# Kernel optimization log

Measured on AMD Instinct MI355X. Metric: run time of the kernel, lower is better.

Reference implementation:

```python
import jax, jax.numpy as jnp
import numpy as np

H = 12   # num_attention_heads
T = 8    # sample_num (frames)
D = 768  # hidden_size


def ln(x, g, b, eps=1e-12):
    m = x.mean(-1, keepdims=True)
    v = x.var(-1, keepdims=True)
    return (x - m) / jnp.sqrt(v + eps) * g + b


def attn(q, k, v):
    # q: [..., Q, Dh], k/v: [..., K, Dh]
    d = q.shape[-1]
    s = jnp.einsum('...qd,...kd->...qk', q, k) / jnp.sqrt(jnp.asarray(d, q.dtype))
    a = jax.nn.softmax(s, axis=-1)
    return jnp.einsum('...qk,...kd->...qd', a, v)


def mha_divided(x, Wq, bq, Wk, bk, Wv, bv, Wo, bo, mode):
    B, S, Dm = x.shape
    Dh = Dm // H
    P = (S - 1) // T

    def proj(W, b):
        return (x @ W + b).reshape(B, S, H, Dh).transpose(0, 2, 1, 3)  # [B,H,S,Dh]

    q, k, v = proj(Wq, bq), proj(Wk, bk), proj(Wv, bv)

    # cls token attends over the full sequence
    cls_ctx = attn(q[:, :, 0:1], k, v)                       # [B,H,1,Dh]
    cls_out = cls_ctx.transpose(0, 2, 1, 3).reshape(B, 1, Dm) @ Wo + bo

    qp = q[:, :, 1:].reshape(B, H, T, P, Dh)
    kp = k[:, :, 1:].reshape(B, H, T, P, Dh)
    vp = v[:, :, 1:].reshape(B, H, T, P, Dh)
    kc, vc = k[:, :, 0], v[:, :, 0]                          # [B,H,Dh]

    if mode == 'time':
        # each patch attends over [cls] + same patch across T frames
        qt = qp.transpose(0, 1, 3, 2, 4)                     # [B,H,P,T,Dh]
        kt = jnp.concatenate([jnp.broadcast_to(kc[:, :, None, None], (B, H, P, 1, Dh)),
                              kp.transpose(0, 1, 3, 2, 4)], axis=3)  # [B,H,P,T+1,Dh]
        vt = jnp.concatenate([jnp.broadcast_to(vc[:, :, None, None], (B, H, P, 1, Dh)),
                              vp.transpose(0, 1, 3, 2, 4)], axis=3)
        ctx = attn(qt, kt, vt)                               # [B,H,P,T,Dh]
        out = ctx.transpose(0, 3, 2, 1, 4).reshape(B, T * P, Dm)  # [B,T,P,H,Dh]
    else:  # 'space': each frame attends over [cls] + P patches in that frame
        kt = jnp.concatenate([jnp.broadcast_to(kc[:, :, None, None], (B, H, T, 1, Dh)), kp], axis=3)
        vt = jnp.concatenate([jnp.broadcast_to(vc[:, :, None, None], (B, H, T, 1, Dh)), vp], axis=3)
        ctx = attn(qp, kt, vt)                               # [B,H,T,P,Dh]
        out = ctx.transpose(0, 2, 3, 1, 4).reshape(B, T * P, Dm)
    out = out @ Wo + bo
    return jnp.concatenate([cls_out, out], axis=1)


def _forward(hidden_states,
             t_Wq, t_bq, t_Wk, t_bk, t_Wv, t_bv, t_Wo, t_bo,
             s_Wq, s_bq, s_Wk, s_bk, s_Wv, s_bv, s_Wo, s_bo,
             W1, b1, W2, b2,
             ln1_g, ln1_b, ln2_g, ln2_b, ln3_g, ln3_b):
    x = hidden_states
    # divided time attention
    x = x + mha_divided(ln(x, ln1_g, ln1_b), t_Wq, t_bq, t_Wk, t_bk, t_Wv, t_bv, t_Wo, t_bo, 'time')
    # divided space attention
    x = x + mha_divided(ln(x, ln2_g, ln2_b), s_Wq, s_bq, s_Wk, s_bk, s_Wv, s_bv, s_Wo, s_bo, 'space')
    # feed-forward with exact (erf) GELU
    h = ln(x, ln3_g, ln3_b)
    x = x + jax.nn.gelu(h @ W1 + b1, approximate=False) @ W2 + b2
    return x


def setup_inputs() -> dict:
    key = jax.random.key(0)
    ks = jax.random.split(key, 16)

    def w(k, shape, s=0.02):
        return jax.random.normal(k, shape, jnp.float32) * s

    B, S = 8, 1 + T * 196
    inp = {"hidden_states": jax.random.normal(ks[0], (B, S, D), jnp.float32)}
    names = ["t_Wq", "t_Wk", "t_Wv", "t_Wo", "s_Wq", "s_Wk", "s_Wv", "s_Wo"]
    for i, n in enumerate(names):
        inp[n] = w(ks[1 + i], (D, D))
        inp[n.replace("W", "b")] = jnp.zeros((D,), jnp.float32)
    inp["W1"] = w(ks[9], (D, 4 * D)); inp["b1"] = jnp.zeros((4 * D,), jnp.float32)
    inp["W2"] = w(ks[10], (4 * D, D)); inp["b2"] = jnp.zeros((D,), jnp.float32)
    for i in (1, 2, 3):
        inp[f"ln{i}_g"] = jnp.ones((D,), jnp.float32)
        inp[f"ln{i}_b"] = jnp.zeros((D,), jnp.float32)
    return inp


def reference(hidden_states,
              t_Wq, t_bq, t_Wk, t_bk, t_Wv, t_bv, t_Wo, t_bo,
              s_Wq, s_bq, s_Wk, s_bk, s_Wv, s_bv, s_Wo, s_bo,
              W1, b1, W2, b2,
              ln1_g, ln1_b, ln2_g, ln2_b, ln3_g, ln3_b):
    return _forward(hidden_states,
                    t_Wq, t_bq, t_Wk, t_bk, t_Wv, t_bv, t_Wo, t_bo,
                    s_Wq, s_bq, s_Wk, s_bk, s_Wv, s_bv, s_Wo, s_bo,
                    W1, b1, W2, b2,
                    ln1_g, ln1_b, ln2_g, ln2_b, ln3_g, ln3_b)
```

## Files before the change

### kernel.cpp

```cpp
#include <hip/hip_runtime.h>

#define BQ   8
#define SQ   1569
#define BS   12552
#define DM   768
#define NH   12
#define DH   64
#define TT   8
#define PP   196
#define D4   3072
#define QKVN 2304
#define CCH  24
#define CKEY 66
#define MB_PAD 104

typedef _Float16 f16;
typedef _Float16 f16x8 __attribute__((ext_vector_type(8)));
typedef float    f32x4 __attribute__((ext_vector_type(4)));
typedef unsigned long long u64;

#define AS1 __attribute__((address_space(1)))
#define AS3 __attribute__((address_space(3)))

#define Y_OFF    0ULL
#define QKV_OFF  19279872ULL
#define CTX_OFF  77119488ULL
#define H_OFF    19279872ULL
#define W_OFF    96399360ULL

__global__ __launch_bounds__(256) void ln_kernel(const float* __restrict__ x,
                                                 const float* __restrict__ g,
                                                 const float* __restrict__ bta,
                                                 f16* __restrict__ y) {
    int row = blockIdx.x * 4 + (threadIdx.x >> 6);
    int lane = threadIdx.x & 63;
    if (row >= BS) return;
    const float* xr = x + (u64)row * DM;
    float v[12];
    float s = 0.f, s2 = 0.f;
#pragma unroll
    for (int i = 0; i < 12; i++) { v[i] = xr[lane + i * 64]; s += v[i]; s2 += v[i] * v[i]; }
#pragma unroll
    for (int m = 1; m < 64; m <<= 1) { s += __shfl_xor(s, m, 64); s2 += __shfl_xor(s2, m, 64); }
    float mean = s * (1.f / 768.f);
    float var  = s2 * (1.f / 768.f) - mean * mean;
    float rstd = rsqrtf(var + 1e-12f);
    f16* yr = y + (u64)row * DM;
#pragma unroll
    for (int i = 0; i < 12; i++) {
        int c = lane + i * 64;
        yr[c] = (f16)((v[i] - mean) * rstd * g[c] + bta[c]);
    }
}

__global__ __launch_bounds__(256) void transpose_kernel(const float* __restrict__ src,
                                                        f16* __restrict__ dst,
                                                        int R, int C) {
    __shared__ float tile[32][33];
    int bx = blockIdx.x * 32;
    int by = blockIdx.y * 32;
    int tx = threadIdx.x & 31, ty = threadIdx.x >> 5;
#pragma unroll
    for (int i = 0; i < 4; i++) {
        int r = by + ty + i * 8, c = bx + tx;
        if (r < R && c < C) tile[ty + i * 8][tx] = src[(u64)r * C + c];
    }
    __syncthreads();
#pragma unroll
    for (int i = 0; i < 4; i++) {
        int c = bx + ty + i * 8, r = by + tx;
        if (c < C && r < R) dst[(u64)c * R + r] = (f16)tile[tx][ty + i * 8];
    }
}

__global__ __launch_bounds__(256) void bias3_kernel(const float* __restrict__ a,
                                                    const float* __restrict__ b,
                                                    const float* __restrict__ c,
                                                    float* __restrict__ dst) {
    int i = blockIdx.x * 256 + threadIdx.x;
    if (i < 768) { dst[i] = a[i]; dst[i + 768] = b[i]; dst[i + 1536] = c[i]; }
}

template <int NOUT, bool GELU, bool RESID, bool OUTF16>
__global__ __launch_bounds__(256, 5) void gemm_kernel(const f16* __restrict__ A,
                                                      const f16* __restrict__ Bt,
                                                      const float* __restrict__ bias,
                                                      const float* __restrict__ resid,
                                                      float* __restrict__ Cf,
                                                      f16* __restrict__ Ch,
                                                      int K) {
    __shared__ __align__(16) f16 As[2][128 * 32];
    __shared__ __align__(16) f16 Bs[2][128 * 32];
    int id = blockIdx.x;
    int mb = id % MB_PAD, nb = id / MB_PAD;
    if (mb >= 99) return;
    int tid  = threadIdx.x;
    int lane = tid & 63, wave = tid >> 6;
    int wm = wave >> 1, wn = wave & 1;
    int m0 = mb * 128, n0 = nb * 128;
    int l15 = lane & 15, quad = lane >> 4;

    int r0   = wave * 16 + (lane >> 2);
    int coff = (lane & 3) * 8;
    const f16* ag0 = A + (u64)(m0 + r0) * K + coff;
    const f16* ag1 = A + (u64)(m0 + r0 + 64) * K + coff;
    bool av0 = (m0 + r0) < BS, av1 = (m0 + r0 + 64) < BS;
    const f16* bg0 = Bt + (u64)(n0 + r0) * K + coff;
    const f16* bg1 = Bt + (u64)(n0 + r0 + 64) * K + coff;
    int lofs = wave * 1024;

    f32x4 acc[4][4];
#pragma unroll
    for (int i = 0; i < 4; i++)
#pragma unroll
        for (int j = 0; j < 4; j++)
#pragma unroll
            for (int r = 0; r < 4; r++) acc[i][j][r] = 0.f;

    if (av0) __builtin_amdgcn_global_load_lds((const AS1 void*)ag0, (AS3 void*)((AS3 char*)&As[0][0] + lofs), 16, 0, 0);
    if (av1) __builtin_amdgcn_global_load_lds((const AS1 void*)ag1, (AS3 void*)((AS3 char*)&As[0][0] + lofs + 4096), 16, 0, 0);
    __builtin_amdgcn_global_load_lds((const AS1 void*)bg0, (AS3 void*)((AS3 char*)&Bs[0][0] + lofs), 16, 0, 0);
    __builtin_amdgcn_global_load_lds((const AS1 void*)bg1, (AS3 void*)((AS3 char*)&Bs[0][0] + lofs + 4096), 16, 0, 0);
    ag0 += 32; ag1 += 32; bg0 += 32; bg1 += 32;

    int nit = K >> 5;
    for (int it = 0; it < nit; it++) {
        __syncthreads();
        int buf = it & 1;
        if (it + 1 < nit) {
            int nb2 = buf ^ 1;
            if (av0) __builtin_amdgcn_global_load_lds((const AS1 void*)ag0, (AS3 void*)((AS3 char*)&As[nb2][0] + lofs), 16, 0, 0);
            if (av1) __builtin_amdgcn_global_load_lds((const AS1 void*)ag1, (AS3 void*)((AS3 char*)&As[nb2][0] + lofs + 4096), 16, 0, 0);
            __builtin_amdgcn_global_load_lds((const AS1 void*)bg0, (AS3 void*)((AS3 char*)&Bs[nb2][0] + lofs), 16, 0, 0);
            __builtin_amdgcn_global_load_lds((const AS1 void*)bg1, (AS3 void*)((AS3 char*)&Bs[nb2][0] + lofs + 4096), 16, 0, 0);
            ag0 += 32; ag1 += 32; bg0 += 32; bg1 += 32;
        }
        f16x8 af[4], bf[4];
#pragma unroll
        for (int i = 0; i < 4; i++)
            af[i] = *(const f16x8*)(&As[buf][(wm * 64 + i * 16 + l15) * 32 + quad * 8]);
#pragma unroll
        for (int j = 0; j < 4; j++)
            bf[j] = *(const f16x8*)(&Bs[buf][(wn * 64 + j * 16 + l15) * 32 + quad * 8]);
#pragma unroll
        for (int i = 0; i < 4; i++)
#pragma unroll
            for (int j = 0; j < 4; j++)
                acc[i][j] = __builtin_amdgcn_mfma_f32_16x16x32_f16(af[i], bf[j], acc[i][j], 0, 0, 0);
    }

#pragma unroll
    for (int i = 0; i < 4; i++) {
#pragma unroll
        for (int j = 0; j < 4; j++) {
            int col = n0 + wn * 64 + j * 16 + l15;
            float bv = bias[col];
#pragma unroll
            for (int r = 0; r < 4; r++) {
                int row = m0 + wm * 64 + i * 16 + quad * 4 + r;
                if (row < BS) {
                    float v = acc[i][j][r] + bv;
                    if (GELU) {
                        float u = 0.7978845608028654f * (v + 0.044715f * v * v * v);
                        float e = __builtin_exp2f(-2.885390081777927f * u);
                        v = v / (1.f + e);
                    }
                    if (RESID) v += resid[(u64)row * NOUT + col];
                    if (OUTF16) Ch[(u64)row * NOUT + col] = (f16)v;
                    else        Cf[(u64)row * NOUT + col] = v;
                }
            }
        }
    }
}

__global__ __launch_bounds__(256) void time_attn_kernel(const f16* __restrict__ qkv,
                                                        f16* __restrict__ ctx) {
    int w = blockIdx.x * 4 + (threadIdx.x >> 6);
    int lane = threadIdx.x & 63;
    int b = w / (NH * PP);
    int rem = w % (NH * PP);
    int h = rem / PP, p = rem % PP;
    u64 bb = (u64)b * SQ;
    int hoff = h * 64 + lane;

    float qv[TT], kv[9], vv[9];
#pragma unroll
    for (int t = 0; t < TT; t++) qv[t] = (float)qkv[(bb + 1 + t * PP + p) * QKVN + hoff];
    kv[0] = (float)qkv[bb * QKVN + 768 + hoff];
    vv[0] = (float)qkv[bb * QKVN + 1536 + hoff];
#pragma unroll
    for (int j = 1; j <= TT; j++) {
        u64 ro = (bb + 1 + (u64)(j - 1) * PP + p) * QKVN;
        kv[j] = (float)qkv[ro + 768 + hoff];
        vv[j] = (float)qkv[ro + 1536 + hoff];
    }
#pragma unroll
    for (int t = 0; t < TT; t++) {
        float s[9];
#pragma unroll
        for (int j = 0; j < 9; j++) {
            float ps = qv[t] * kv[j];
#pragma unroll
            for (int m = 1; m < 64; m <<= 1) ps += __shfl_xor(ps, m, 64);
            s[j] = ps * 0.125f;
        }
        float mx = s[0];
#pragma unroll
        for (int j = 1; j < 9; j++) mx = fmaxf(mx, s[j]);
        float sum = 0.f;
#pragma unroll
        for (int j = 0; j < 9; j++) { s[j] = expf(s[j] - mx); sum += s[j]; }
        float o = 0.f;
#pragma unroll
        for (int j = 0; j < 9; j++) o += s[j] * vv[j];
        o /= sum;
        ctx[(bb + 1 + (u64)t * PP + p) * DM + h * 64 + lane] = (f16)o;
    }
}

__global__ __launch_bounds__(256) void cls_part_kernel(const f16* __restrict__ qkv,
                                                       float* __restrict__ part) {
    int g = blockIdx.x;
    int c = g % CCH, bh = g / CCH;
    int b = bh / NH, h = bh % NH;
    u64 bb = (u64)b * SQ;
    int tid = threadIdx.x, lane = tid & 63, wave = tid >> 6;
    __shared__ float sc[CKEY];
    __shared__ float accbuf[4][64];
    __shared__ float lbuf[4];
    __shared__ float mxs;
    float qd = (float)qkv[bb * QKVN + h * 64 + lane];
    int j0 = c * CKEY;
    int cnt = SQ - j0; if (cnt > CKEY) cnt = CKEY;
    for (int jj = wave; jj < cnt; jj += 4) {
        float p = qd * (float)qkv[(bb + j0 + jj) * QKVN + 768 + h * 64 + lane];
#pragma unroll
        for (int m = 1; m < 64; m <<= 1) p += __shfl_xor(p, m, 64);
        if (lane == 0) sc[jj] = p * 0.125f;
    }
    __syncthreads();
    if (wave == 0) {
        float m = -1e30f;
        for (int j = lane; j < cnt; j += 64) m = fmaxf(m, sc[j]);
#pragma unroll
        for (int s = 1; s < 64; s <<= 1) m = fmaxf(m, __shfl_xor(m, s, 64));
        if (lane == 0) mxs = m;
    }
    __syncthreads();
    float mx = mxs;
    float acc = 0.f, l = 0.f;
    for (int jj = wave; jj < cnt; jj += 4) {
        float w = expf(sc[jj] - mx);
        l += w;
        acc += w * (float)qkv[(bb + j0 + jj) * QKVN + 1536 + h * 64 + lane];
    }
    accbuf[wave][lane] = acc;
    if (lane == 0) lbuf[wave] = l;
    __syncthreads();
    if (tid < 64) {
        float a = accbuf[0][tid] + accbuf[1][tid] + accbuf[2][tid] + accbuf[3][tid];
        float* pb = part + ((u64)bh * CCH + c) * 66;
        if (tid == 0) { pb[0] = mxs; pb[1] = lbuf[0] + lbuf[1] + lbuf[2] + lbuf[3]; }
        pb[2 + tid] = a;
    }
}

__global__ __launch_bounds__(256) void cls_comb_kernel(const float* __restrict__ part,
                                                       f16* __restrict__ ctx) {
    int w = blockIdx.x * 4 + (threadIdx.x >> 6);
    int lane = threadIdx.x & 63;
    if (w >= BQ * NH) return;
    int b = w / NH, h = w % NH;
    const float* pb = part + (u64)w * CCH * 66;
    float m = (lane < CCH) ? pb[lane * 66] : -1e30f;
#pragma unroll
    for (int s = 1; s < 64; s <<= 1) m = fmaxf(m, __shfl_xor(m, s, 64));
    float l = (lane < CCH) ? pb[lane * 66 + 1] * expf(pb[lane * 66] - m) : 0.f;
#pragma unroll
    for (int s = 1; s < 64; s <<= 1) l += __shfl_xor(l, s, 64);
    float o = 0.f;
    for (int j = 0; j < CCH; j++) {
        float mj = pb[j * 66];
        o += pb[j * 66 + 2 + lane] * expf(mj - m);
    }
    ctx[((u64)b * SQ) * DM + h * 64 + lane] = (f16)(o / l);
}

__global__ __launch_bounds__(256) void space_attn_kernel(const f16* __restrict__ qkv,
                                                         f16* __restrict__ ctx) {
    int g = blockIdx.x;
    int b = g / (NH * TT);
    int rem = g % (NH * TT);
    int h = rem / TT, t = rem % TT;
    __shared__ __align__(16) f16 Vt[64 * 232];
    __shared__ __align__(16) f16 Ps[4 * 16 * 232];
    u64 bb = (u64)b * SQ;
    int tid = threadIdx.x, lane = tid & 63, wave = tid >> 6;
    int l15 = lane & 15, quad = lane >> 4;

    for (int i = tid; i < 4 * 16 * 232 * 2 / 16; i += 256)
        ((uint4*)Ps)[i] = make_uint4(0u, 0u, 0u, 0u);

    for (int idx = tid; idx < 232 * 8; idx += 256) {
        int c8 = idx / 232;
        int j  = idx - c8 * 232;
        int c  = c8 * 8;
        uint4 vraw = make_uint4(0u, 0u, 0u, 0u);
        if (j < 197) {
            int tok = (j == 0) ? 0 : (1 + t * PP + (j - 1));
            vraw = *(const uint4*)(qkv + (bb + tok) * QKVN + 1536 + h * 64 + c);
        }
        f16x8 vv = *(f16x8*)&vraw;
#pragma unroll
        for (int e = 0; e < 8; e++) Vt[(c + e) * 232 + j] = vv[e];
    }
    __syncthreads();

    f16* myP = Ps + wave * 16 * 232;
    for (int qt = wave; qt < 13; qt += 4) {
        int mloc = qt * 16 + l15;
        int mc = mloc > 195 ? 195 : mloc;
        const f16* qr = qkv + (bb + 1 + (u64)t * PP + mc) * QKVN + h * 64;
        f16x8 qa0 = *(const f16x8*)(qr + quad * 8);
        f16x8 qa1 = *(const f16x8*)(qr + 32 + quad * 8);

        f32x4 s[13];
#pragma unroll
        for (int nt = 0; nt < 13; nt++) { s[nt][0] = 0.f; s[nt][1] = 0.f; s[nt][2] = 0.f; s[nt][3] = 0.f; }
#pragma unroll
        for (int nt = 0; nt < 13; nt++) {
            int n = nt * 16 + l15;
            int ncl = n > 196 ? 196 : n;
            int tok = (ncl == 0) ? 0 : (1 + t * PP + (ncl - 1));
            const f16* kr = qkv + (bb + tok) * QKVN + 768 + h * 64;
            f16x8 kb0 = *(const f16x8*)(kr + quad * 8);
            f16x8 kb1 = *(const f16x8*)(kr + 32 + quad * 8);
            s[nt] = __builtin_amdgcn_mfma_f32_16x16x32_f16(qa0, kb0, s[nt], 0, 0, 0);
            s[nt] = __builtin_amdgcn_mfma_f32_16x16x32_f16(qa1, kb1, s[nt], 0, 0, 0);
        }
        if (l15 >= 5) { s[12][0] = -1e30f; s[12][1] = -1e30f; s[12][2] = -1e30f; s[12][3] = -1e30f; }

        float mx[4] = {-1e30f, -1e30f, -1e30f, -1e30f};
#pragma unroll
        for (int nt = 0; nt < 13; nt++)
#pragma unroll
            for (int r = 0; r < 4; r++) mx[r] = fmaxf(mx[r], s[nt][r]);
#pragma unroll
        for (int m = 1; m < 16; m <<= 1)
#pragma unroll
            for (int r = 0; r < 4; r++) mx[r] = fmaxf(mx[r], __shfl_xor(mx[r], m, 64));

        float sum[4] = {0.f, 0.f, 0.f, 0.f};
#pragma unroll
        for (int nt = 0; nt < 13; nt++)
#pragma unroll
            for (int r = 0; r < 4; r++) {
                float p = exp2f((s[nt][r] - mx[r]) * 0.18033688011112042f);
                s[nt][r] = p;
                sum[r] += p;
            }
#pragma unroll
        for (int m = 1; m < 16; m <<= 1)
#pragma unroll
            for (int r = 0; r < 4; r++) sum[r] += __shfl_xor(sum[r], m, 64);

#pragma unroll
        for (int nt = 0; nt < 13; nt++)
#pragma unroll
            for (int r = 0; r < 4; r++)
                myP[(quad * 4 + r) * 232 + nt * 16 + l15] = (f16)s[nt][r];

        f32x4 o[4];
#pragma unroll
        for (int n2 = 0; n2 < 4; n2++) { o[n2][0] = 0.f; o[n2][1] = 0.f; o[n2][2] = 0.f; o[n2][3] = 0.f; }
#pragma unroll
        for (int kc = 0; kc < 7; kc++) {
            f16x8 pa = *(const f16x8*)(&myP[l15 * 232 + kc * 32 + quad * 8]);
#pragma unroll
            for (int n2 = 0; n2 < 4; n2++) {
                f16x8 vb = *(const f16x8*)(&Vt[(n2 * 16 + l15) * 232 + kc * 32 + quad * 8]);
                o[n2] = __builtin_amdgcn_mfma_f32_16x16x32_f16(pa, vb, o[n2], 0, 0, 0);
            }
        }

        float inv[4];
#pragma unroll
        for (int r = 0; r < 4; r++) inv[r] = 1.f / sum[r];
#pragma unroll
        for (int n2 = 0; n2 < 4; n2++)
#pragma unroll
            for (int r = 0; r < 4; r++) {
                int m = qt * 16 + quad * 4 + r;
                if (m < PP)
                    ctx[(bb + 1 + (u64)t * PP + m) * DM + h * 64 + n2 * 16 + l15] = (f16)(o[n2][r] * inv[r]);
            }
    }
}

extern "C" void kernel_launch(void* const* d_in, const int* in_sizes, int n_in,
                              void* d_out, int out_size, void* d_ws, size_t ws_size,
                              hipStream_t stream) {
    const float* x_in  = (const float*)d_in[0];
    const float* t_Wq  = (const float*)d_in[1];
    const float* t_bq  = (const float*)d_in[2];
    const float* t_Wk  = (const float*)d_in[3];
    const float* t_bk  = (const float*)d_in[4];
    const float* t_Wv  = (const float*)d_in[5];
    const float* t_bv  = (const float*)d_in[6];
    const float* t_Wo  = (const float*)d_in[7];
    const float* t_bo  = (const float*)d_in[8];
    const float* s_Wq  = (const float*)d_in[9];
    const float* s_bq  = (const float*)d_in[10];
    const float* s_Wk  = (const float*)d_in[11];
    const float* s_bk  = (const float*)d_in[12];
    const float* s_Wv  = (const float*)d_in[13];
    const float* s_bv  = (const float*)d_in[14];
    const float* s_Wo  = (const float*)d_in[15];
    const float* s_bo  = (const float*)d_in[16];
    const float* W1    = (const float*)d_in[17];
    const float* b1    = (const float*)d_in[18];
    const float* W2    = (const float*)d_in[19];
    const float* b2    = (const float*)d_in[20];
    const float* ln1g  = (const float*)d_in[21];
    const float* ln1b  = (const float*)d_in[22];
    const float* ln2g  = (const float*)d_in[23];
    const float* ln2b  = (const float*)d_in[24];
    const float* ln3g  = (const float*)d_in[25];
    const float* ln3b  = (const float*)d_in[26];

    char* ws = (char*)d_ws;
    f16* y    = (f16*)(ws + Y_OFF);
    f16* qkv  = (f16*)(ws + QKV_OFF);
    f16* ctx  = (f16*)(ws + CTX_OFF);
    f16* hbuf = (f16*)(ws + H_OFF);
    float* clsP = (float*)(ws + Y_OFF);
    char* wreg = ws + W_OFF;
    f16* tQKV  = (f16*)(wreg);
    f16* tWoT  = (f16*)(wreg + 3538944);
    f16* sQKV  = (f16*)(wreg + 4718592);
    f16* sWoT  = (f16*)(wreg + 8257536);
    f16* W1T   = (f16*)(wreg + 9437184);
    f16* W2T   = (f16*)(wreg + 14155776);
    float* tBias = (float*)(wreg + 18874368);
    float* sBias = (float*)(wreg + 18883584);
    float* xcur  = (float*)d_out;

    dim3 tb(256);
    transpose_kernel<<<dim3(24, 24), tb, 0, stream>>>(t_Wq, tQKV, 768, 768);
    transpose_kernel<<<dim3(24, 24), tb, 0, stream>>>(t_Wk, tQKV + 768 * 768, 768, 768);
    transpose_kernel<<<dim3(24, 24), tb, 0, stream>>>(t_Wv, tQKV + 2 * 768 * 768, 768, 768);
    transpose_kernel<<<dim3(24, 24), tb, 0, stream>>>(t_Wo, tWoT, 768, 768);
    transpose_kernel<<<dim3(24, 24), tb, 0, stream>>>(s_Wq, sQKV, 768, 768);
    transpose_kernel<<<dim3(24, 24), tb, 0, stream>>>(s_Wk, sQKV + 768 * 768, 768, 768);
    transpose_kernel<<<dim3(24, 24), tb, 0, stream>>>(s_Wv, sQKV + 2 * 768 * 768, 768, 768);
    transpose_kernel<<<dim3(24, 24), tb, 0, stream>>>(s_Wo, sWoT, 768, 768);
    transpose_kernel<<<dim3(96, 24), tb, 0, stream>>>(W1, W1T, 768, 3072);
    transpose_kernel<<<dim3(24, 96), tb, 0, stream>>>(W2, W2T, 3072, 768);
    bias3_kernel<<<3, tb, 0, stream>>>(t_bq, t_bk, t_bv, tBias);
    bias3_kernel<<<3, tb, 0, stream>>>(s_bq, s_bk, s_bv, sBias);

    ln_kernel<<<3138, tb, 0, stream>>>(x_in, ln1g, ln1b, y);
    gemm_kernel<QKVN, false, false, true><<<MB_PAD * 18, tb, 0, stream>>>(y, tQKV, tBias, nullptr, nullptr, qkv, 768);
    time_attn_kernel<<<4704, tb, 0, stream>>>(qkv, ctx);
    cls_part_kernel<<<BQ * NH * CCH, tb, 0, stream>>>(qkv, clsP);
    cls_comb_kernel<<<24, tb, 0, stream>>>(clsP, ctx);
    gemm_kernel<DM, false, true, false><<<MB_PAD * 6, tb, 0, stream>>>(ctx, tWoT, t_bo, x_in, xcur, nullptr, 768);

    ln_kernel<<<3138, tb, 0, stream>>>(xcur, ln2g, ln2b, y);
    gemm_kernel<QKVN, false, false, true><<<MB_PAD * 18, tb, 0, stream>>>(y, sQKV, sBias, nullptr, nullptr, qkv, 768);
    space_attn_kernel<<<768, tb, 0, stream>>>(qkv, ctx);
    cls_part_kernel<<<BQ * NH * CCH, tb, 0, stream>>>(qkv, clsP);
    cls_comb_kernel<<<24, tb, 0, stream>>>(clsP, ctx);
    gemm_kernel<DM, false, true, false><<<MB_PAD * 6, tb, 0, stream>>>(ctx, sWoT, s_bo, xcur, xcur, nullptr, 768);

    ln_kernel<<<3138, tb, 0, stream>>>(xcur, ln3g, ln3b, y);
    gemm_kernel<D4, true, false, true><<<MB_PAD * 24, tb, 0, stream>>>(y, W1T, b1, nullptr, nullptr, hbuf, 768);
    gemm_kernel<DM, false, true, false><<<MB_PAD * 6, tb, 0, stream>>>(hbuf, W2T, b2, xcur, xcur, nullptr, 3072);
}
```

Before: 880.7 us.

## Triple-buffer GEMM LDS pipeline with XOR swizzle and explicit vmcnt waits

The GEMM main loop moves from double to triple buffering. Tiles are prefetched two iterations ahead, and each iteration waits with explicit s_waitcnt vmcnt plus a raw barrier instead of __syncthreads, which allows more loads in flight. Global-to-LDS column offsets and the LDS read offsets get a matching XOR swizzle to reduce bank conflicts, and out-of-range A rows are clamped instead of skipped. LDS use grows by half and the occupancy hint drops from 5 to 3 blocks per CU, trading occupancy for deeper latency hiding.

```diff
diff --git a/kernel.cpp b/kernel.cpp
--- a/kernel.cpp
+++ b/kernel.cpp
@@ -82,15 +82,15 @@
 }
 
 template <int NOUT, bool GELU, bool RESID, bool OUTF16>
-__global__ __launch_bounds__(256, 5) void gemm_kernel(const f16* __restrict__ A,
+__global__ __launch_bounds__(256, 3) void gemm_kernel(const f16* __restrict__ A,
                                                       const f16* __restrict__ Bt,
                                                       const float* __restrict__ bias,
                                                       const float* __restrict__ resid,
                                                       float* __restrict__ Cf,
                                                       f16* __restrict__ Ch,
                                                       int K) {
-    __shared__ __align__(16) f16 As[2][128 * 32];
-    __shared__ __align__(16) f16 Bs[2][128 * 32];
+    __shared__ __align__(16) f16 As[3][128 * 32];
+    __shared__ __align__(16) f16 Bs[3][128 * 32];
     int id = blockIdx.x;
     int mb = id % MB_PAD, nb = id / MB_PAD;
     if (mb >= 99) return;
@@ -101,14 +101,25 @@
     int l15 = lane & 15, quad = lane >> 4;
 
     int r0   = wave * 16 + (lane >> 2);
-    int coff = (lane & 3) * 8;
-    const f16* ag0 = A + (u64)(m0 + r0) * K + coff;
-    const f16* ag1 = A + (u64)(m0 + r0 + 64) * K + coff;
-    bool av0 = (m0 + r0) < BS, av1 = (m0 + r0 + 64) < BS;
+    int coff = (((lane & 3) ^ ((lane >> 3) & 3))) * 8;
+    int ra0 = m0 + r0;       if (ra0 > BS - 1) ra0 = BS - 1;
+    int ra1 = m0 + r0 + 64;  if (ra1 > BS - 1) ra1 = BS - 1;
+    const f16* ag0 = A + (u64)ra0 * K + coff;
+    const f16* ag1 = A + (u64)ra1 * K + coff;
     const f16* bg0 = Bt + (u64)(n0 + r0) * K + coff;
     const f16* bg1 = Bt + (u64)(n0 + r0 + 64) * K + coff;
     int lofs = wave * 1024;
 
+    int gsw = (quad ^ ((l15 >> 1) & 3)) * 8;
+
+#define STAGE(BUF, KT) { \
+    u64 _ko = (u64)(KT) * 32; \
+    __builtin_amdgcn_global_load_lds((const AS1 void*)(ag0 + _ko), (AS3 void*)((AS3 char*)&As[BUF][0] + lofs), 16, 0, 0); \
+    __builtin_amdgcn_global_load_lds((const AS1 void*)(ag1 + _ko), (AS3 void*)((AS3 char*)&As[BUF][0] + lofs + 4096), 16, 0, 0); \
+    __builtin_amdgcn_global_load_lds((const AS1 void*)(bg0 + _ko), (AS3 void*)((AS3 char*)&Bs[BUF][0] + lofs), 16, 0, 0); \
+    __builtin_amdgcn_global_load_lds((const AS1 void*)(bg1 + _ko), (AS3 void*)((AS3 char*)&Bs[BUF][0] + lofs + 4096), 16, 0, 0); \
+}
+
     f32x4 acc[4][4];
 #pragma unroll
     for (int i = 0; i < 4; i++)
@@ -117,37 +128,35 @@
 #pragma unroll
             for (int r = 0; r < 4; r++) acc[i][j][r] = 0.f;
 
-    if (av0) __builtin_amdgcn_global_load_lds((const AS1 void*)ag0, (AS3 void*)((AS3 char*)&As[0][0] + lofs), 16, 0, 0);
-    if (av1) __builtin_amdgcn_global_load_lds((const AS1 void*)ag1, (AS3 void*)((AS3 char*)&As[0][0] + lofs + 4096), 16, 0, 0);
-    __builtin_amdgcn_global_load_lds((const AS1 void*)bg0, (AS3 void*)((AS3 char*)&Bs[0][0] + lofs), 16, 0, 0);
-    __builtin_amdgcn_global_load_lds((const AS1 void*)bg1, (AS3 void*)((AS3 char*)&Bs[0][0] + lofs + 4096), 16, 0, 0);
-    ag0 += 32; ag1 += 32; bg0 += 32; bg1 += 32;
+    STAGE(0, 0);
+    STAGE(1, 1);
 
     int nit = K >> 5;
+    int cbuf = 0, sbuf = 2;
     for (int it = 0; it < nit; it++) {
-        __syncthreads();
-        int buf = it & 1;
-        if (it + 1 < nit) {
-            int nb2 = buf ^ 1;
-            if (av0) __builtin_amdgcn_global_load_lds((const AS1 void*)ag0, (AS3 void*)((AS3 char*)&As[nb2][0] + lofs), 16, 0, 0);
-            if (av1) __builtin_amdgcn_global_load_lds((const AS1 void*)ag1, (AS3 void*)((AS3 char*)&As[nb2][0] + lofs + 4096), 16, 0, 0);
-            __builtin_amdgcn_global_load_lds((const AS1 void*)bg0, (AS3 void*)((AS3 char*)&Bs[nb2][0] + lofs), 16, 0, 0);
-            __builtin_amdgcn_global_load_lds((const AS1 void*)bg1, (AS3 void*)((AS3 char*)&Bs[nb2][0] + lofs + 4096), 16, 0, 0);
-            ag0 += 32; ag1 += 32; bg0 += 32; bg1 += 32;
-        }
+        if (it + 1 < nit) { asm volatile("s_waitcnt vmcnt(4)"); }
+        else              { asm volatile("s_waitcnt vmcnt(0)"); }
+        __builtin_amdgcn_s_barrier();
+        __builtin_amdgcn_sched_barrier(0);
+        if (it + 2 < nit) STAGE(sbuf, it + 2);
+
         f16x8 af[4], bf[4];
 #pragma unroll
         for (int i = 0; i < 4; i++)
-            af[i] = *(const f16x8*)(&As[buf][(wm * 64 + i * 16 + l15) * 32 + quad * 8]);
+            af[i] = *(const f16x8*)(&As[cbuf][(wm * 64 + i * 16 + l15) * 32 + gsw]);
 #pragma unroll
         for (int j = 0; j < 4; j++)
-            bf[j] = *(const f16x8*)(&Bs[buf][(wn * 64 + j * 16 + l15) * 32 + quad * 8]);
+            bf[j] = *(const f16x8*)(&Bs[cbuf][(wn * 64 + j * 16 + l15) * 32 + gsw]);
 #pragma unroll
         for (int i = 0; i < 4; i++)
 #pragma unroll
             for (int j = 0; j < 4; j++)
                 acc[i][j] = __builtin_amdgcn_mfma_f32_16x16x32_f16(af[i], bf[j], acc[i][j], 0, 0, 0);
-    }
+
+        cbuf = (cbuf == 2) ? 0 : cbuf + 1;
+        sbuf = (sbuf == 2) ? 0 : sbuf + 1;
+    }
+#undef STAGE
 
 #pragma unroll
     for (int i = 0; i < 4; i++) {
```

After: 904.9 us. +2.7%, slower.
